# Kernel tuning notes

Measured on AMD Instinct MI355X. Metric: run time of the kernel, lower is better.

## Reference

```python
import jax, jax.numpy as jnp
import numpy as np

B, N, DIN, D, E, STEP = 4, 1024, 256, 256, 5, 5


def setup_inputs() -> dict:
    key = jax.random.key(0)
    ks = jax.random.split(key, 14)
    s = 0.02  # weight init scale
    inp = {
        "node_features": jax.random.normal(ks[0], (B, N, DIN), dtype=jnp.float32),
        # dense per-edge-type adjacency; scaled so messages stay in a sane range
        "adj_matrices": jax.random.uniform(ks[1], (B, E, N, N), dtype=jnp.float32) * (2.0 / N),
        "fc_in_w": jax.random.normal(ks[2], (D, DIN), dtype=jnp.float32) * s,
        "fc_in_b": jnp.zeros((D,), dtype=jnp.float32),
        "edge_w": jax.random.normal(ks[3], (E, D, D), dtype=jnp.float32) * s,
        "edge_b": jax.random.normal(ks[4], (E, D), dtype=jnp.float32) * s,
        "gru_w_ih": jax.random.normal(ks[5], (3 * D, D), dtype=jnp.float32) * s,
        "gru_w_hh": jax.random.normal(ks[6], (3 * D, D), dtype=jnp.float32) * s,
        "gru_b_ih": jnp.zeros((3 * D,), dtype=jnp.float32),
        "gru_b_hh": jnp.zeros((3 * D,), dtype=jnp.float32),
        "conv1_w": jax.random.normal(ks[7], (D, D), dtype=jnp.float32) * s,
        "conv1_b": jnp.zeros((D,), dtype=jnp.float32),
        "conv2_w": jax.random.normal(ks[8], (D, D), dtype=jnp.float32) * s,
        "conv2_b": jnp.zeros((D,), dtype=jnp.float32),
    }
    return inp


def _gru_cell(x, h, w_ih, w_hh, b_ih, b_hh):
    # torch GRUCell: gates ordered [r, z, n]
    gi = x @ w_ih.T + b_ih  # [B*N, 3D]
    gh = h @ w_hh.T + b_hh
    ir, iz, inn = jnp.split(gi, 3, axis=-1)
    hr, hz, hn = jnp.split(gh, 3, axis=-1)
    r = jax.nn.sigmoid(ir + hr)
    z = jax.nn.sigmoid(iz + hz)
    n = jnp.tanh(inn + r * hn)
    return (1.0 - z) * n + z * h


def reference(node_features, adj_matrices, fc_in_w, fc_in_b, edge_w, edge_b,
              gru_w_ih, gru_w_hh, gru_b_ih, gru_b_hh,
              conv1_w, conv1_b, conv2_w, conv2_b):
    h = node_features @ fc_in_w.T + fc_in_b  # [B, N, D]
    sum_edge_b = jnp.sum(edge_b, axis=0)  # accumulated biases over edge types
    for _ in range(STEP):
        # messages per edge type: adj_e @ h  -> [B, E, N, D]
        msgs = jnp.einsum('benm,bmd->bend', adj_matrices, h)
        # per-edge-type linear (y = x @ W_e.T) then accumulate over edge types
        acc = jnp.einsum('bend,ekd->bnk', msgs, edge_w) + sum_edge_b  # [B, N, D]
        h = _gru_cell(acc, h, gru_w_ih, gru_w_hh, gru_b_ih, gru_b_hh)
    node_states = h  # [B, N, D]
    # conv1d with kernel_size=1 over node axis == per-node linear on channels
    attn_weights = jax.nn.sigmoid(node_states @ conv1_w.T + conv1_b)  # [B, N, D]
    feats = jnp.tanh(node_states @ conv2_w.T + conv2_b)  # [B, N, D]
    graph_embedding = jnp.sum(attn_weights * feats, axis=1)  # sum over nodes -> [B, D]
    attn_map = jnp.mean(attn_weights, axis=2)  # mean over channels -> [B, N]
    return (graph_embedding, node_states, attn_map)
```

## Files before the change

kernel.cpp:

```cpp
#include <hip/hip_runtime.h>
#include <hip/hip_bf16.h>
#include <cstdint>


typedef __attribute__((ext_vector_type(8))) short bf16x8;
typedef __attribute__((ext_vector_type(4))) float f32x4;

__device__ __forceinline__ float bf2f(__hip_bfloat16 x) { return __bfloat162float(x); }
__device__ __forceinline__ __hip_bfloat16 f2bf(float x) { return __float2bfloat16(x); }
__device__ __forceinline__ short f2bs(float x) {
  __hip_bfloat16 h = __float2bfloat16(x);
  return *reinterpret_cast<short*>(&h);
}
__device__ __forceinline__ float s2f(short x) {
  __hip_bfloat16 h = *reinterpret_cast<__hip_bfloat16*>(&x);
  return __bfloat162float(h);
}

__device__ __forceinline__ bf16x8 ld8_ext(const void* base, long off, bool f32) {
  if (f32) {
    const float* p = (const float*)base + off;
    bf16x8 r;
#pragma unroll
    for (int i = 0; i < 8; ++i) r[i] = f2bs(p[i]);
    return r;
  }
  return *(const bf16x8*)((const __hip_bfloat16*)base + off);
}

__device__ __forceinline__ bf16x8 ld8_sum5(const __hip_bfloat16* part, int row, int k) {
  const long base = (long)row * 256 + (long)(row >> 10) * 1048576 + k;
  float s[8] = {0.f, 0.f, 0.f, 0.f, 0.f, 0.f, 0.f, 0.f};
#pragma unroll
  for (int e = 0; e < 5; ++e) {
    bf16x8 v = *(const bf16x8*)(part + base + e * 262144);
#pragma unroll
    for (int j = 0; j < 8; ++j) s[j] += s2f(v[j]);
  }
  bf16x8 r;
#pragma unroll
  for (int j = 0; j < 8; ++j) r[j] = f2bs(s[j]);
  return r;
}

__global__ void detect_dtype(const uint32_t* __restrict__ raw, int* __restrict__ flag) {
  __shared__ int cnt;
  if (threadIdx.x == 0) cnt = 0;
  __syncthreads();
  int c = 0;
  for (int i = threadIdx.x; i < 512; i += 256) {
    uint32_t byte = (raw[i] >> 8) & 0xFF;
    if (byte >= 0x28 && byte <= 0x40) ++c;
  }
  atomicAdd(&cnt, c);
  __syncthreads();
  if (threadIdx.x == 0) *flag = (cnt < 300) ? 1 : 0;
}

__global__ void prep_pool(const void* fcb, const void* bih, const void* bhh,
                          const void* c1b, const void* c2b, const void* edgeb,
                          const int* __restrict__ flag,
                          float* __restrict__ pool, float* __restrict__ ge,
                          float* __restrict__ am32) {
  const bool f32 = (*flag != 0);
  for (int t = threadIdx.x; t < 2560; t += 256) {
    const void* p; int i;
    if (t < 256)       { p = fcb;  i = t; }
    else if (t < 1024) { p = bih;  i = t - 256; }
    else if (t < 1792) { p = bhh;  i = t - 1024; }
    else if (t < 2048) { p = c1b;  i = t - 1792; }
    else if (t < 2304) { p = c2b;  i = t - 2048; }
    else {
      int k = t - 2304; float s = 0.f;
      for (int e = 0; e < 5; ++e)
        s += f32 ? ((const float*)edgeb)[e * 256 + k]
                 : bf2f(((const __hip_bfloat16*)edgeb)[e * 256 + k]);
      pool[t] = s; continue;
    }
    pool[t] = f32 ? ((const float*)p)[i] : bf2f(((const __hip_bfloat16*)p)[i]);
  }
  for (int t = threadIdx.x; t < 1024; t += 256) ge[t] = 0.f;
  for (int t = threadIdx.x; t < 4096; t += 256) am32[t] = 0.f;
}

__global__ void bias_gi_k(const float* __restrict__ pool,
                          const __hip_bfloat16* __restrict__ wih,
                          float* __restrict__ out) {
  const int n = blockIdx.x * 256 + threadIdx.x;
  if (n >= 768) return;
  float s = pool[256 + n];
  for (int k = 0; k < 256; ++k) s += pool[2304 + k] * bf2f(wih[n * 256 + k]);
  out[n] = s;
}

__global__ void wcvt_all(const void* fcw, const void* edw, const void* wih,
                         const void* whh, const void* c1w, const void* c2w,
                         const int* __restrict__ flag, __hip_bfloat16* __restrict__ dst) {
  const bool f32 = (*flag != 0);
  const int i = blockIdx.x * 256 + threadIdx.x;
  const void* src; int off;
  if      (i < 65536)  { src = fcw; off = i; }
  else if (i < 393216) { src = edw; off = i - 65536; }
  else if (i < 589824) { src = wih; off = i - 393216; }
  else if (i < 786432) { src = whh; off = i - 589824; }
  else if (i < 851968) { src = c1w; off = i - 786432; }
  else                 { src = c2w; off = i - 851968; }
  dst[i] = f32 ? f2bf(((const float*)src)[off])
               : ((const __hip_bfloat16*)src)[off];
}

__global__ void adj_cvt(const void* __restrict__ src, const int* __restrict__ flag,
                        __hip_bfloat16* __restrict__ dst) {
  const bool f32 = (*flag != 0);
  const long i = ((long)blockIdx.x * 256 + threadIdx.x) * 8;
  bf16x8 r;
  if (f32) {
    const float* p = (const float*)src + i;
#pragma unroll
    for (int j = 0; j < 8; ++j) r[j] = f2bs(p[j]);
  } else {
    r = *(const bf16x8*)((const __hip_bfloat16*)src + i);
  }
  *(bf16x8*)(dst + i) = r;
}

__global__ void sum_part(const __hip_bfloat16* __restrict__ part,
                         __hip_bfloat16* __restrict__ out) {
  const int t = blockIdx.x * 256 + threadIdx.x;
  const int row = t >> 5;
  const int k = (t & 31) * 8;
  const long base = (long)row * 256 + (long)(row >> 10) * 1048576 + k;
  float s[8] = {0.f, 0.f, 0.f, 0.f, 0.f, 0.f, 0.f, 0.f};
#pragma unroll
  for (int e = 0; e < 5; ++e) {
    bf16x8 v = *(const bf16x8*)(part + base + e * 262144);
#pragma unroll
    for (int j = 0; j < 8; ++j) s[j] += s2f(v[j]);
  }
  bf16x8 r;
#pragma unroll
  for (int j = 0; j < 8; ++j) r[j] = f2bs(s[j]);
  *(bf16x8*)(out + (long)row * 256 + k) = r;
}

template<bool HAS_BIAS, bool DUAL>
__global__ __launch_bounds__(256)
void gemm_bt128(const __hip_bfloat16* __restrict__ A, const __hip_bfloat16* __restrict__ Bt,
                const float* __restrict__ bias, __hip_bfloat16* __restrict__ C,
                const __hip_bfloat16* __restrict__ A2, const __hip_bfloat16* __restrict__ Bt2,
                const float* __restrict__ bias2, __hip_bfloat16* __restrict__ C2,
                int K, int lda, int ldb, int ldc,
                long aBatch, int zdivA, int zmodA,
                long bBatch, int zdivB, int zmodB,
                long cBatch, int zdivC, int zSplit)
{
  __shared__ __align__(16) __hip_bfloat16 sA[128 * 64];
  __shared__ __align__(16) __hip_bfloat16 sB[64 * 64];
  const int t = threadIdx.x;
  const int w = t >> 6;
  const int l = t & 63;
  const int m0 = blockIdx.x * 128;
  const int n0 = blockIdx.y * 64;
  int z = blockIdx.z;

  const __hip_bfloat16* Au = A; const __hip_bfloat16* Btu = Bt;
  const float* biasu = bias; __hip_bfloat16* Cu = C;
  if (DUAL && z >= zSplit) { Au = A2; Btu = Bt2; biasu = bias2; Cu = C2; z -= zSplit; }

  const __hip_bfloat16* Ab = Au + (long)((z / zdivA) % zmodA) * aBatch;
  const __hip_bfloat16* Bb = Btu + (long)((z / zdivB) % zmodB) * bBatch;

  int sra[4], sca[4];
#pragma unroll
  for (int i = 0; i < 4; ++i) {
    const int p = t + 256 * i;
    sra[i] = p >> 3;
    sca[i] = (p & 7) ^ (sra[i] & 7);
  }
  const int p0 = t, p1 = t + 256;
  const int sr0 = p0 >> 3, sc0 = (p0 & 7) ^ (sr0 & 7);
  const int sr1 = p1 >> 3, sc1 = (p1 & 7) ^ (sr1 & 7);

  f32x4 acc[2][4];
#pragma unroll
  for (int i = 0; i < 2; ++i)
#pragma unroll
    for (int j = 0; j < 4; ++j) acc[i][j] = (f32x4){0.f, 0.f, 0.f, 0.f};

  const int r15 = l & 15;
  const int quad = l >> 4;

  for (int k0 = 0; k0 < K; k0 += 64) {
    bf16x8 av[4];
#pragma unroll
    for (int i = 0; i < 4; ++i)
      av[i] = *(const bf16x8*)(Ab + (long)(m0 + sra[i]) * lda + (k0 + sca[i] * 8));
    bf16x8 b0 = *(const bf16x8*)(Bb + (long)(n0 + sr0) * ldb + (k0 + sc0 * 8));
    bf16x8 b1 = *(const bf16x8*)(Bb + (long)(n0 + sr1) * ldb + (k0 + sc1 * 8));
    __syncthreads();
#pragma unroll
    for (int i = 0; i < 4; ++i) *(bf16x8*)(sA + (t + 256 * i) * 8) = av[i];
    *(bf16x8*)(sB + p0 * 8) = b0;
    *(bf16x8*)(sB + p1 * 8) = b1;
    __syncthreads();
#pragma unroll
    for (int ks = 0; ks < 2; ++ks) {
      const int cg = ks * 4 + quad;
      bf16x8 aF[2], bF[4];
#pragma unroll
      for (int mi = 0; mi < 2; ++mi) {
        const int row = mi * 64 + w * 16 + r15;
        aF[mi] = *(const bf16x8*)(sA + row * 64 + ((cg ^ (row & 7)) * 8));
      }
#pragma unroll
      for (int ni = 0; ni < 4; ++ni) {
        const int nrow = ni * 16 + r15;
        bF[ni] = *(const bf16x8*)(sB + nrow * 64 + ((cg ^ (nrow & 7)) * 8));
      }
#pragma unroll
      for (int mi = 0; mi < 2; ++mi)
#pragma unroll
        for (int ni = 0; ni < 4; ++ni)
          acc[mi][ni] = __builtin_amdgcn_mfma_f32_16x16x32_bf16(
              aF[mi], bF[ni], acc[mi][ni], 0, 0, 0);
    }
  }

  const long cOff = (long)(z / zdivC) * cBatch;
#pragma unroll
  for (int mi = 0; mi < 2; ++mi) {
#pragma unroll
    for (int ni = 0; ni < 4; ++ni) {
      const int n = n0 + ni * 16 + r15;
      float bv = 0.f;
      if (HAS_BIAS) bv = biasu[n];
#pragma unroll
      for (int r = 0; r < 4; ++r) {
        const int m = m0 + mi * 64 + w * 16 + quad * 4 + r;
        Cu[cOff + (long)m * ldc + n] = f2bf(acc[mi][ni][r] + bv);
      }
    }
  }
}

template<int OUT_MODE, bool HAS_BIAS, int A_MODE, bool DUAL>
__global__ __launch_bounds__(256)
void gemm_bt(const void* __restrict__ A, const __hip_bfloat16* __restrict__ Bt,
             const float* __restrict__ bias, void* __restrict__ Cp,
             const void* __restrict__ A2, const __hip_bfloat16* __restrict__ Bt2,
             const float* __restrict__ bias2, void* __restrict__ Cp2,
             const int* __restrict__ flag,
             int Kg, int ngrp, int lda, int ldb, int ldc,
             long aBatch, int zdivA, int zmodA,
             long bBatch, int zdivB, int zmodB,
             long cBatch, int zdivC, long aGrp, long bGrp, int zSplit)
{
  __shared__ __align__(16) __hip_bfloat16 sA[64 * 64];
  __shared__ __align__(16) __hip_bfloat16 sB[64 * 64];
  const bool af32 = (A_MODE == 1) ? (*flag != 0) : false;
  const int t = threadIdx.x;
  const int w = t >> 6;
  const int l = t & 63;
  const int m0 = blockIdx.x * 64;
  const int n0 = blockIdx.y * 64;
  int z = blockIdx.z;

  const void* Au = A; const __hip_bfloat16* Btu = Bt;
  const float* biasu = bias; void* Cpu = Cp;
  bool second = false;
  if (DUAL && z >= zSplit) {
    Au = A2; Btu = Bt2; biasu = bias2; Cpu = Cp2; z -= zSplit; second = true;
  }

  const long aOff = (long)((z / zdivA) % zmodA) * aBatch;
  const __hip_bfloat16* Bb = Btu + (long)((z / zdivB) % zmodB) * bBatch;

  const int p0 = t, p1 = t + 256;
  const int sr0 = p0 >> 3, sc0 = (p0 & 7) ^ (sr0 & 7);
  const int sr1 = p1 >> 3, sc1 = (p1 & 7) ^ (sr1 & 7);

  f32x4 acc[4];
#pragma unroll
  for (int i = 0; i < 4; ++i) acc[i] = (f32x4){0.f, 0.f, 0.f, 0.f};

  const int mrow = w * 16 + (l & 15);
  const int quad = l >> 4;

  for (int g = 0; g < ngrp; ++g) {
    const long aG = aOff + (long)g * aGrp;
    const __hip_bfloat16* Bg = Bb + (long)g * bGrp;
    for (int k0 = 0; k0 < Kg; k0 += 64) {
      bf16x8 a0, a1;
      if (A_MODE == 2 && !second) {
        a0 = ld8_sum5((const __hip_bfloat16*)Au, m0 + sr0, k0 + sc0 * 8);
        a1 = ld8_sum5((const __hip_bfloat16*)Au, m0 + sr1, k0 + sc1 * 8);
      } else if (A_MODE == 1) {
        a0 = ld8_ext(Au, aG + (long)(m0 + sr0) * lda + (k0 + sc0 * 8), af32);
        a1 = ld8_ext(Au, aG + (long)(m0 + sr1) * lda + (k0 + sc1 * 8), af32);
      } else {
        const __hip_bfloat16* Ab = (const __hip_bfloat16*)Au;
        a0 = *(const bf16x8*)(Ab + aG + (long)(m0 + sr0) * lda + (k0 + sc0 * 8));
        a1 = *(const bf16x8*)(Ab + aG + (long)(m0 + sr1) * lda + (k0 + sc1 * 8));
      }
      bf16x8 b0 = *(const bf16x8*)(Bg + (long)(n0 + sr0) * ldb + (k0 + sc0 * 8));
      bf16x8 b1 = *(const bf16x8*)(Bg + (long)(n0 + sr1) * ldb + (k0 + sc1 * 8));
      __syncthreads();
      *(bf16x8*)(sA + p0 * 8) = a0;
      *(bf16x8*)(sA + p1 * 8) = a1;
      *(bf16x8*)(sB + p0 * 8) = b0;
      *(bf16x8*)(sB + p1 * 8) = b1;
      __syncthreads();
#pragma unroll
      for (int ks = 0; ks < 2; ++ks) {
        const int cg = ks * 4 + quad;
        bf16x8 af = *(const bf16x8*)(sA + mrow * 64 + ((cg ^ (mrow & 7)) * 8));
#pragma unroll
        for (int t4 = 0; t4 < 4; ++t4) {
          const int nrow = t4 * 16 + (l & 15);
          bf16x8 bfr = *(const bf16x8*)(sB + nrow * 64 + ((cg ^ (nrow & 7)) * 8));
          acc[t4] = __builtin_amdgcn_mfma_f32_16x16x32_bf16(af, bfr, acc[t4], 0, 0, 0);
        }
      }
    }
  }

  const long cOff = (long)(z / zdivC) * cBatch;
#pragma unroll
  for (int t4 = 0; t4 < 4; ++t4) {
    const int n = n0 + t4 * 16 + (l & 15);
    float bv = 0.f;
    if (HAS_BIAS) bv = biasu[n];
#pragma unroll
    for (int r = 0; r < 4; ++r) {
      const int m = m0 + w * 16 + quad * 4 + r;
      const float v = acc[t4][r] + bv;
      if (OUT_MODE == 0)
        ((__hip_bfloat16*)Cpu)[cOff + (long)m * ldc + n] = f2bf(v);
      else
        ((float*)Cpu)[cOff + (long)m * ldc + n] = v;
    }
  }
}

__global__ void gru_gate8(const __hip_bfloat16* __restrict__ gi,
                          const __hip_bfloat16* __restrict__ gh,
                          __hip_bfloat16* __restrict__ hbf,
                          void* __restrict__ ns_out, const int* __restrict__ flag)
{
  const int t = blockIdx.x * 256 + threadIdx.x;
  const int m = t >> 5;
  const int k = (t & 31) * 8;
  const long gb = (long)m * 768 + k;
  bf16x8 vir = *(const bf16x8*)(gi + gb);
  bf16x8 viz = *(const bf16x8*)(gi + gb + 256);
  bf16x8 vin = *(const bf16x8*)(gi + gb + 512);
  bf16x8 vhr = *(const bf16x8*)(gh + gb);
  bf16x8 vhz = *(const bf16x8*)(gh + gb + 256);
  bf16x8 vhn = *(const bf16x8*)(gh + gb + 512);
  const long hidx = (long)m * 256 + k;
  bf16x8 vh = *(const bf16x8*)(hbf + hidx);
  bf16x8 out;
  float hf[8];
#pragma unroll
  for (int j = 0; j < 8; ++j) {
    const float r = 1.f / (1.f + __expf(-(s2f(vir[j]) + s2f(vhr[j]))));
    const float zz = 1.f / (1.f + __expf(-(s2f(viz[j]) + s2f(vhz[j]))));
    const float nn = tanhf(s2f(vin[j]) + r * s2f(vhn[j]));
    hf[j] = (1.f - zz) * nn + zz * s2f(vh[j]);
    out[j] = f2bs(hf[j]);
  }
  *(bf16x8*)(hbf + hidx) = out;
  if (ns_out) {
    if (*flag) {
      float* o = (float*)ns_out + 1024 + hidx;
#pragma unroll
      for (int j = 0; j < 8; ++j) o[j] = hf[j];
    } else {
      *(bf16x8*)((__hip_bfloat16*)ns_out + 1024 + hidx) = out;
    }
  }
}

__global__ __launch_bounds__(256)
void conv_fused(const __hip_bfloat16* __restrict__ hbf,
                const __hip_bfloat16* __restrict__ c1w,
                const __hip_bfloat16* __restrict__ c2w,
                const float* __restrict__ pool,
                float* __restrict__ geg, float* __restrict__ am32)
{
  __shared__ __align__(16) __hip_bfloat16 sA[64 * 64];
  __shared__ __align__(16) __hip_bfloat16 sB1[64 * 64];
  __shared__ __align__(16) __hip_bfloat16 sB2[64 * 64];
  __shared__ float sge[64];
  __shared__ float sam[64];
  const int t = threadIdx.x, w = t >> 6, l = t & 63;
  const int m0 = blockIdx.x * 64, n0 = blockIdx.y * 64;
  if (t < 64) { sge[t] = 0.f; sam[t] = 0.f; }
  const int p0 = t, p1 = t + 256;
  const int sr0 = p0 >> 3, sc0 = (p0 & 7) ^ (sr0 & 7);
  const int sr1 = p1 >> 3, sc1 = (p1 & 7) ^ (sr1 & 7);
  f32x4 a1[4], a2[4];
#pragma unroll
  for (int i = 0; i < 4; ++i) { a1[i] = (f32x4){0,0,0,0}; a2[i] = (f32x4){0,0,0,0}; }
  const int mrow = w * 16 + (l & 15);
  const int quad = l >> 4;
  for (int k0 = 0; k0 < 256; k0 += 64) {
    bf16x8 va0 = *(const bf16x8*)(hbf + (long)(m0 + sr0) * 256 + (k0 + sc0 * 8));
    bf16x8 va1 = *(const bf16x8*)(hbf + (long)(m0 + sr1) * 256 + (k0 + sc1 * 8));
    bf16x8 vb0 = *(const bf16x8*)(c1w + (long)(n0 + sr0) * 256 + (k0 + sc0 * 8));
    bf16x8 vb1 = *(const bf16x8*)(c1w + (long)(n0 + sr1) * 256 + (k0 + sc1 * 8));
    bf16x8 vc0 = *(const bf16x8*)(c2w + (long)(n0 + sr0) * 256 + (k0 + sc0 * 8));
    bf16x8 vc1 = *(const bf16x8*)(c2w + (long)(n0 + sr1) * 256 + (k0 + sc1 * 8));
    __syncthreads();
    *(bf16x8*)(sA + p0 * 8) = va0;  *(bf16x8*)(sA + p1 * 8) = va1;
    *(bf16x8*)(sB1 + p0 * 8) = vb0; *(bf16x8*)(sB1 + p1 * 8) = vb1;
    *(bf16x8*)(sB2 + p0 * 8) = vc0; *(bf16x8*)(sB2 + p1 * 8) = vc1;
    __syncthreads();
#pragma unroll
    for (int ks = 0; ks < 2; ++ks) {
      const int cg = ks * 4 + quad;
      bf16x8 af = *(const bf16x8*)(sA + mrow * 64 + ((cg ^ (mrow & 7)) * 8));
#pragma unroll
      for (int t4 = 0; t4 < 4; ++t4) {
        const int nrow = t4 * 16 + (l & 15);
        bf16x8 b1f = *(const bf16x8*)(sB1 + nrow * 64 + ((cg ^ (nrow & 7)) * 8));
        bf16x8 b2f = *(const bf16x8*)(sB2 + nrow * 64 + ((cg ^ (nrow & 7)) * 8));
        a1[t4] = __builtin_amdgcn_mfma_f32_16x16x32_bf16(af, b1f, a1[t4], 0, 0, 0);
        a2[t4] = __builtin_amdgcn_mfma_f32_16x16x32_bf16(af, b2f, a2[t4], 0, 0, 0);
      }
    }
  }
  float asum[4] = {0.f, 0.f, 0.f, 0.f};
#pragma unroll
  for (int t4 = 0; t4 < 4; ++t4) {
    const int n = n0 + t4 * 16 + (l & 15);
    const float bb1 = pool[1792 + n], bb2 = pool[2048 + n];
    float g = 0.f;
#pragma unroll
    for (int r = 0; r < 4; ++r) {
      const float av = 1.f / (1.f + __expf(-(a1[t4][r] + bb1)));
      const float fv = tanhf(a2[t4][r] + bb2);
      g += av * fv;
      asum[r] += av;
    }
    atomicAdd(&sge[t4 * 16 + (l & 15)], g);
  }
#pragma unroll
  for (int r = 0; r < 4; ++r) atomicAdd(&sam[w * 16 + quad * 4 + r], asum[r]);
  __syncthreads();
  if (t < 64) atomicAdd(&geg[(m0 >> 10) * 256 + n0 + t], sge[t]);
  else if (t < 128) atomicAdd(&am32[m0 + (t - 64)], sam[t - 64]);
}

__global__ void finish_out(const float* __restrict__ ge, const float* __restrict__ am32,
                           void* __restrict__ dout, const int* __restrict__ flag)
{
  const int t = blockIdx.x * 256 + threadIdx.x;
  const bool f32 = (*flag != 0);
  if (t < 1024) {
    if (f32) ((float*)dout)[t] = ge[t];
    else     ((__hip_bfloat16*)dout)[t] = f2bf(ge[t]);
  } else {
    const float v = am32[t - 1024] * (1.f / 256.f);
    if (f32) ((float*)dout)[1049600 + t - 1024] = v;
    else     ((__hip_bfloat16*)dout)[1049600 + t - 1024] = f2bf(v);
  }
}

extern "C" void kernel_launch(void* const* d_in, const int* in_sizes, int n_in,
                              void* d_out, int out_size, void* d_ws, size_t ws_size,
                              hipStream_t stream) {
  (void)in_sizes; (void)n_in; (void)out_size;
  const void* node_f = d_in[0];
  const void* adj    = d_in[1];
  const void* fc_w   = d_in[2];
  const void* fc_b   = d_in[3];
  const void* edge_w = d_in[4];
  const void* edge_b = d_in[5];
  const void* w_ih   = d_in[6];
  const void* w_hh   = d_in[7];
  const void* b_ih   = d_in[8];
  const void* b_hh   = d_in[9];
  const void* c1w    = d_in[10];
  const void* c1b    = d_in[11];
  const void* c2w    = d_in[12];
  const void* c2b    = d_in[13];

  char* ws = (char*)d_ws;
  const size_t MB = (size_t)1 << 20;
  int*            flag = (int*)(ws);
  float*          bp   = (float*)(ws + 256);
  float*          ge   = (float*)(ws + 14336);
  float*          am32 = (float*)(ws + 18432);
  __hip_bfloat16* wbf  = (__hip_bfloat16*)(ws + 34816);
  __hip_bfloat16* hbf  = (__hip_bfloat16*)(ws + 1869824);
  char*           S    = ws + 3966976;
  __hip_bfloat16* heT  = (__hip_bfloat16*)(S);
  __hip_bfloat16* part = (__hip_bfloat16*)(S + 10 * MB);
  __hip_bfloat16* gi   = (__hip_bfloat16*)(S + 20 * MB);
  __hip_bfloat16* gh   = (__hip_bfloat16*)(S + 26 * MB);
  __hip_bfloat16* spt  = (__hip_bfloat16*)(S + 32 * MB);
  __hip_bfloat16* adjb = (__hip_bfloat16*)(ws + 40 * MB);

  const bool has_split = ws_size >= 38 * MB;
  const bool has_adjb  = ws_size >= 81 * MB;

  detect_dtype<<<1, 256, 0, stream>>>((const uint32_t*)adj, flag);
  prep_pool<<<1, 256, 0, stream>>>(fc_b, b_ih, b_hh, c1b, c2b, edge_b, flag, bp, ge, am32);
  wcvt_all<<<3584, 256, 0, stream>>>(fc_w, edge_w, w_ih, w_hh, c1w, c2w, flag, wbf);
  bias_gi_k<<<3, 256, 0, stream>>>(bp, wbf + 393216, bp + 2560);
  if (has_adjb) adj_cvt<<<10240, 256, 0, stream>>>(adj, flag, adjb);

  gemm_bt<0, true, 1, false><<<dim3(64, 4, 1), 256, 0, stream>>>(
      node_f, wbf + 0, bp + 0, hbf, nullptr, nullptr, nullptr, nullptr, flag,
      256, 1, 256, 256, 256, 0, 1, 1, 0, 1, 1, 0, 1, 0, 0, 0);

  for (int s = 0; s < 5; ++s) {
    if (has_adjb) {
      gemm_bt128<false, false><<<dim3(2, 16, 20), 256, 0, stream>>>(
          wbf + 65536, hbf, nullptr, heT, nullptr, nullptr, nullptr, nullptr,
          256, 256, 256, 1024,
          65536, 1, 5,
          262144, 5, 4,
          262144, 1, 0);
      gemm_bt128<false, false><<<dim3(8, 4, 20), 256, 0, stream>>>(
          adjb, heT, nullptr, part, nullptr, nullptr, nullptr, nullptr,
          1024, 1024, 1024, 256,
          1048576, 1, 20,
          262144, 1, 20,
          262144, 1, 0);
      sum_part<<<512, 256, 0, stream>>>(part, spt);
      gemm_bt128<true, true><<<dim3(32, 12, 2), 256, 0, stream>>>(
          spt, wbf + 393216, bp + 2560, gi,
          hbf, wbf + 589824, bp + 1024, gh,
          256, 256, 256, 768,
          0, 1, 1, 0, 1, 1, 0, 1, 1);
    } else if (has_split) {
      gemm_bt<0, false, 0, false><<<dim3(4, 16, 20), 256, 0, stream>>>(
          wbf + 65536, hbf, nullptr, heT, nullptr, nullptr, nullptr, nullptr, flag,
          256, 1, 256, 256, 1024,
          65536, 1, 5, 262144, 5, 4,
          262144, 1, 0, 0, 0);
      gemm_bt<0, false, 1, false><<<dim3(16, 4, 20), 256, 0, stream>>>(
          adj, heT, nullptr, part, nullptr, nullptr, nullptr, nullptr, flag,
          1024, 1, 1024, 1024, 256,
          1048576, 1, 20, 262144, 1, 20,
          262144, 1, 0, 0, 0);
      gemm_bt<0, true, 2, true><<<dim3(64, 12, 2), 256, 0, stream>>>(
          part, wbf + 393216, bp + 2560, gi,
          hbf,  wbf + 589824, bp + 1024, gh, flag,
          256, 1, 256, 256, 768, 0, 1, 1, 0, 1, 1, 0, 1, 0, 0, 1);
    } else {
      gemm_bt<0, false, 0, false><<<dim3(4, 16, 20), 256, 0, stream>>>(
          wbf + 65536, hbf, nullptr, heT, nullptr, nullptr, nullptr, nullptr, flag,
          256, 1, 256, 256, 1024,
          65536, 1, 5, 262144, 5, 4,
          262144, 1, 0, 0, 0);
      gemm_bt<0, true, 1, false><<<dim3(16, 4, 4), 256, 0, stream>>>(
          adj, heT, bp + 2304, part, nullptr, nullptr, nullptr, nullptr, flag,
          1024, 5, 1024, 1024, 256,
          (long)5 * 1048576, 1, 4, (long)5 * 262144, 1, 4,
          262144, 1, 1048576, 262144, 0);
      gemm_bt<0, true, 0, true><<<dim3(64, 12, 2), 256, 0, stream>>>(
          part, wbf + 393216, bp + 256, gi,
          hbf,  wbf + 589824, bp + 1024, gh, flag,
          256, 1, 256, 256, 768, 0, 1, 1, 0, 1, 1, 0, 1, 0, 0, 1);
    }
    gru_gate8<<<512, 256, 0, stream>>>(gi, gh, hbf,
                                       (s == 4) ? d_out : nullptr, flag);
  }

  conv_fused<<<dim3(64, 4), 256, 0, stream>>>(hbf, wbf + 786432, wbf + 851968,
                                              bp, ge, am32);
  finish_out<<<20, 256, 0, stream>>>(ge, am32, d_out, flag);
}
```

Baseline: 449.3 us.

## Fuse partial-sum into gi GEMM with GRU gate, co-schedule adjacency and gh GEMMs

In the adjacency-converted path, the adjacency GEMM and the h·W_hh GEMM now run in one launch that splits blocks by index. A new gi_gate kernel sums the five edge-type partials as it loads them (ld8_sum5), computes all three gate projections per tile, and applies the GRU update in its epilogue. This drops the sum_part kernel, the intermediate spt and gi buffers, and the separate gru_gate8 launch. The cost is more shared memory and accumulators per block in gi_gate and only 256 blocks for that stage, which may limit occupancy.

```diff
diff --git a/kernel.cpp b/kernel.cpp
--- a/kernel.cpp
+++ b/kernel.cpp
@@ -124,25 +124,6 @@
   *(bf16x8*)(dst + i) = r;
 }
 
-__global__ void sum_part(const __hip_bfloat16* __restrict__ part,
-                         __hip_bfloat16* __restrict__ out) {
-  const int t = blockIdx.x * 256 + threadIdx.x;
-  const int row = t >> 5;
-  const int k = (t & 31) * 8;
-  const long base = (long)row * 256 + (long)(row >> 10) * 1048576 + k;
-  float s[8] = {0.f, 0.f, 0.f, 0.f, 0.f, 0.f, 0.f, 0.f};
-#pragma unroll
-  for (int e = 0; e < 5; ++e) {
-    bf16x8 v = *(const bf16x8*)(part + base + e * 262144);
-#pragma unroll
-    for (int j = 0; j < 8; ++j) s[j] += s2f(v[j]);
-  }
-  bf16x8 r;
-#pragma unroll
-  for (int j = 0; j < 8; ++j) r[j] = f2bs(s[j]);
-  *(bf16x8*)(out + (long)row * 256 + k) = r;
-}
-
 template<bool HAS_BIAS, bool DUAL>
 __global__ __launch_bounds__(256)
 void gemm_bt128(const __hip_bfloat16* __restrict__ A, const __hip_bfloat16* __restrict__ Bt,
@@ -238,6 +219,212 @@
       for (int r = 0; r < 4; ++r) {
         const int m = m0 + mi * 64 + w * 16 + quad * 4 + r;
         Cu[cOff + (long)m * ldc + n] = f2bf(acc[mi][ni][r] + bv);
+      }
+    }
+  }
+}
+
+__global__ __launch_bounds__(256)
+void part_gh(const __hip_bfloat16* __restrict__ adjb,
+             const __hip_bfloat16* __restrict__ heT,
+             __hip_bfloat16* __restrict__ part,
+             const __hip_bfloat16* __restrict__ hbf,
+             const __hip_bfloat16* __restrict__ whh,
+             const float* __restrict__ bhh,
+             __hip_bfloat16* __restrict__ gh)
+{
+  __shared__ __align__(16) __hip_bfloat16 sA[128 * 64];
+  __shared__ __align__(16) __hip_bfloat16 sB[64 * 64];
+  const int t = threadIdx.x;
+  const int w = t >> 6;
+  const int l = t & 63;
+  const int bid = blockIdx.x;
+
+  const __hip_bfloat16* Ab; const __hip_bfloat16* Bb;
+  __hip_bfloat16* Cu; const float* biasu = nullptr;
+  int K, lda, ldb, ldc, m0, n0;
+  bool has_bias;
+  if (bid < 640) {
+    const int z = bid >> 5, rem = bid & 31;
+    m0 = (rem & 7) * 128; n0 = (rem >> 3) * 64;
+    Ab = adjb + (long)z * 1048576; lda = 1024; K = 1024;
+    Bb = heT + (long)z * 262144;  ldb = 1024;
+    Cu = part + (long)z * 262144; ldc = 256;
+    has_bias = false;
+  } else {
+    const int idx = bid - 640;
+    m0 = (idx & 31) * 128; n0 = (idx >> 5) * 64;
+    Ab = hbf; lda = 256; K = 256;
+    Bb = whh; ldb = 256;
+    Cu = gh;  ldc = 768;
+    biasu = bhh; has_bias = true;
+  }
+
+  int sra[4], sca[4];
+#pragma unroll
+  for (int i = 0; i < 4; ++i) {
+    const int p = t + 256 * i;
+    sra[i] = p >> 3;
+    sca[i] = (p & 7) ^ (sra[i] & 7);
+  }
+  const int p0 = t, p1 = t + 256;
+  const int sr0 = p0 >> 3, sc0 = (p0 & 7) ^ (sr0 & 7);
+  const int sr1 = p1 >> 3, sc1 = (p1 & 7) ^ (sr1 & 7);
+
+  f32x4 acc[2][4];
+#pragma unroll
+  for (int i = 0; i < 2; ++i)
+#pragma unroll
+    for (int j = 0; j < 4; ++j) acc[i][j] = (f32x4){0.f, 0.f, 0.f, 0.f};
+
+  const int r15 = l & 15;
+  const int quad = l >> 4;
+
+  for (int k0 = 0; k0 < K; k0 += 64) {
+    bf16x8 av[4];
+#pragma unroll
+    for (int i = 0; i < 4; ++i)
+      av[i] = *(const bf16x8*)(Ab + (long)(m0 + sra[i]) * lda + (k0 + sca[i] * 8));
+    bf16x8 b0 = *(const bf16x8*)(Bb + (long)(n0 + sr0) * ldb + (k0 + sc0 * 8));
+    bf16x8 b1 = *(const bf16x8*)(Bb + (long)(n0 + sr1) * ldb + (k0 + sc1 * 8));
+    __syncthreads();
+#pragma unroll
+    for (int i = 0; i < 4; ++i) *(bf16x8*)(sA + (t + 256 * i) * 8) = av[i];
+    *(bf16x8*)(sB + p0 * 8) = b0;
+    *(bf16x8*)(sB + p1 * 8) = b1;
+    __syncthreads();
+#pragma unroll
+    for (int ks = 0; ks < 2; ++ks) {
+      const int cg = ks * 4 + quad;
+      bf16x8 aF[2], bF[4];
+#pragma unroll
+      for (int mi = 0; mi < 2; ++mi) {
+        const int row = mi * 64 + w * 16 + r15;
+        aF[mi] = *(const bf16x8*)(sA + row * 64 + ((cg ^ (row & 7)) * 8));
+      }
+#pragma unroll
+      for (int ni = 0; ni < 4; ++ni) {
+        const int nrow = ni * 16 + r15;
+        bF[ni] = *(const bf16x8*)(sB + nrow * 64 + ((cg ^ (nrow & 7)) * 8));
+      }
+#pragma unroll
+      for (int mi = 0; mi < 2; ++mi)
+#pragma unroll
+        for (int ni = 0; ni < 4; ++ni)
+          acc[mi][ni] = __builtin_amdgcn_mfma_f32_16x16x32_bf16(
+              aF[mi], bF[ni], acc[mi][ni], 0, 0, 0);
+    }
+  }
+
+#pragma unroll
+  for (int mi = 0; mi < 2; ++mi) {
+#pragma unroll
+    for (int ni = 0; ni < 4; ++ni) {
+      const int n = n0 + ni * 16 + r15;
+      const float bv = has_bias ? biasu[n] : 0.f;
+#pragma unroll
+      for (int r = 0; r < 4; ++r) {
+        const int m = m0 + mi * 64 + w * 16 + quad * 4 + r;
+        Cu[(long)m * ldc + n] = f2bf(acc[mi][ni][r] + bv);
+      }
+    }
+  }
+}
+
+__global__ __launch_bounds__(256)
+void gi_gate(const __hip_bfloat16* __restrict__ part,
+             const __hip_bfloat16* __restrict__ wih,
+             const float* __restrict__ biasgi,
+             const __hip_bfloat16* __restrict__ gh,
+             __hip_bfloat16* __restrict__ hbf,
+             void* __restrict__ ns_out, const int* __restrict__ flag)
+{
+  __shared__ __align__(16) __hip_bfloat16 sA[64 * 64];
+  __shared__ __align__(16) __hip_bfloat16 sB0[64 * 64];
+  __shared__ __align__(16) __hip_bfloat16 sB1[64 * 64];
+  __shared__ __align__(16) __hip_bfloat16 sB2[64 * 64];
+  const int t = threadIdx.x;
+  const int w = t >> 6;
+  const int l = t & 63;
+  const int m0 = (blockIdx.x & 63) * 64;
+  const int n0 = (blockIdx.x >> 6) * 64;
+
+  const int p0 = t, p1 = t + 256;
+  const int sr0 = p0 >> 3, sc0 = (p0 & 7) ^ (sr0 & 7);
+  const int sr1 = p1 >> 3, sc1 = (p1 & 7) ^ (sr1 & 7);
+
+  f32x4 acc[3][4];
+#pragma unroll
+  for (int g = 0; g < 3; ++g)
+#pragma unroll
+    for (int j = 0; j < 4; ++j) acc[g][j] = (f32x4){0.f, 0.f, 0.f, 0.f};
+
+  const int mrow = w * 16 + (l & 15);
+  const int r15 = l & 15;
+  const int quad = l >> 4;
+
+  for (int k0 = 0; k0 < 256; k0 += 64) {
+    bf16x8 a0 = ld8_sum5(part, m0 + sr0, k0 + sc0 * 8);
+    bf16x8 a1 = ld8_sum5(part, m0 + sr1, k0 + sc1 * 8);
+    bf16x8 bg[3][2];
+#pragma unroll
+    for (int g = 0; g < 3; ++g) {
+      bg[g][0] = *(const bf16x8*)(wih + (long)(g * 256 + n0 + sr0) * 256 + (k0 + sc0 * 8));
+      bg[g][1] = *(const bf16x8*)(wih + (long)(g * 256 + n0 + sr1) * 256 + (k0 + sc1 * 8));
+    }
+    __syncthreads();
+    *(bf16x8*)(sA + p0 * 8) = a0;
+    *(bf16x8*)(sA + p1 * 8) = a1;
+    *(bf16x8*)(sB0 + p0 * 8) = bg[0][0]; *(bf16x8*)(sB0 + p1 * 8) = bg[0][1];
+    *(bf16x8*)(sB1 + p0 * 8) = bg[1][0]; *(bf16x8*)(sB1 + p1 * 8) = bg[1][1];
+    *(bf16x8*)(sB2 + p0 * 8) = bg[2][0]; *(bf16x8*)(sB2 + p1 * 8) = bg[2][1];
+    __syncthreads();
+#pragma unroll
+    for (int ks = 0; ks < 2; ++ks) {
+      const int cg = ks * 4 + quad;
+      bf16x8 af = *(const bf16x8*)(sA + mrow * 64 + ((cg ^ (mrow & 7)) * 8));
+#pragma unroll
+      for (int t4 = 0; t4 < 4; ++t4) {
+        const int nrow = t4 * 16 + r15;
+        const int so = nrow * 64 + ((cg ^ (nrow & 7)) * 8);
+        bf16x8 b0f = *(const bf16x8*)(sB0 + so);
+        bf16x8 b1f = *(const bf16x8*)(sB1 + so);
+        bf16x8 b2f = *(const bf16x8*)(sB2 + so);
+        acc[0][t4] = __builtin_amdgcn_mfma_f32_16x16x32_bf16(af, b0f, acc[0][t4], 0, 0, 0);
+        acc[1][t4] = __builtin_amdgcn_mfma_f32_16x16x32_bf16(af, b1f, acc[1][t4], 0, 0, 0);
+        acc[2][t4] = __builtin_amdgcn_mfma_f32_16x16x32_bf16(af, b2f, acc[2][t4], 0, 0, 0);
+      }
+    }
+  }
+
+  const bool f32out = ns_out && (*flag != 0);
+#pragma unroll
+  for (int t4 = 0; t4 < 4; ++t4) {
+    const int n = n0 + t4 * 16 + r15;
+    const float bgr = biasgi[n];
+    const float bgz = biasgi[256 + n];
+    const float bgn = biasgi[512 + n];
+#pragma unroll
+    for (int r = 0; r < 4; ++r) {
+      const int m = m0 + w * 16 + quad * 4 + r;
+      const long gb = (long)m * 768;
+      const float ir = acc[0][t4][r] + bgr;
+      const float iz = acc[1][t4][r] + bgz;
+      const float inn = acc[2][t4][r] + bgn;
+      const float hr = bf2f(gh[gb + n]);
+      const float hz = bf2f(gh[gb + 256 + n]);
+      const float hn = bf2f(gh[gb + 512 + n]);
+      const long hidx = (long)m * 256 + n;
+      const float h = bf2f(hbf[hidx]);
+      const float rr = 1.f / (1.f + __expf(-(ir + hr)));
+      const float zz = 1.f / (1.f + __expf(-(iz + hz)));
+      const float nn = tanhf(inn + rr * hn);
+      const float hnew = (1.f - zz) * nn + zz * h;
+      const __hip_bfloat16 hb = f2bf(hnew);
+      hbf[hidx] = hb;
+      if (ns_out) {
+        if (f32out) ((float*)ns_out)[1024 + hidx] = hnew;
+        else        ((__hip_bfloat16*)ns_out)[1024 + hidx] = hb;
       }
     }
   }
@@ -499,7 +686,6 @@
   __hip_bfloat16* part = (__hip_bfloat16*)(S + 10 * MB);
   __hip_bfloat16* gi   = (__hip_bfloat16*)(S + 20 * MB);
   __hip_bfloat16* gh   = (__hip_bfloat16*)(S + 26 * MB);
-  __hip_bfloat16* spt  = (__hip_bfloat16*)(S + 32 * MB);
   __hip_bfloat16* adjb = (__hip_bfloat16*)(ws + 40 * MB);
 
   const bool has_split = ws_size >= 38 * MB;
@@ -523,18 +709,10 @@
           65536, 1, 5,
           262144, 5, 4,
           262144, 1, 0);
-      gemm_bt128<false, false><<<dim3(8, 4, 20), 256, 0, stream>>>(
-          adjb, heT, nullptr, part, nullptr, nullptr, nullptr, nullptr,
-          1024, 1024, 1024, 256,
-          1048576, 1, 20,
-          262144, 1, 20,
-          262144, 1, 0);
-      sum_part<<<512, 256, 0, stream>>>(part, spt);
-      gemm_bt128<true, true><<<dim3(32, 12, 2), 256, 0, stream>>>(
-          spt, wbf + 393216, bp + 2560, gi,
-          hbf, wbf + 589824, bp + 1024, gh,
-          256, 256, 256, 768,
-          0, 1, 1, 0, 1, 1, 0, 1, 1);
+      part_gh<<<1024, 256, 0, stream>>>(adjb, heT, part,
+                                        hbf, wbf + 589824, bp + 1024, gh);
+      gi_gate<<<256, 256, 0, stream>>>(part, wbf + 393216, bp + 2560, gh, hbf,
+                                       (s == 4) ? d_out : nullptr, flag);
     } else if (has_split) {
       gemm_bt<0, false, 0, false><<<dim3(4, 16, 20), 256, 0, stream>>>(
           wbf + 65536, hbf, nullptr, heT, nullptr, nullptr, nullptr, nullptr, flag,
@@ -550,6 +728,8 @@
           part, wbf + 393216, bp + 2560, gi,
           hbf,  wbf + 589824, bp + 1024, gh, flag,
           256, 1, 256, 256, 768, 0, 1, 1, 0, 1, 1, 0, 1, 0, 0, 1);
+      gru_gate8<<<512, 256, 0, stream>>>(gi, gh, hbf,
+                                         (s == 4) ? d_out : nullptr, flag);
     } else {
       gemm_bt<0, false, 0, false><<<dim3(4, 16, 20), 256, 0, stream>>>(
           wbf + 65536, hbf, nullptr, heT, nullptr, nullptr, nullptr, nullptr, flag,
@@ -565,9 +745,9 @@
           part, wbf + 393216, bp + 256, gi,
           hbf,  wbf + 589824, bp + 1024, gh, flag,
           256, 1, 256, 256, 768, 0, 1, 1, 0, 1, 1, 0, 1, 0, 0, 1);
-    }
-    gru_gate8<<<512, 256, 0, stream>>>(gi, gh, hbf,
-                                       (s == 4) ? d_out : nullptr, flag);
+      gru_gate8<<<512, 256, 0, stream>>>(gi, gh, hbf,
+                                         (s == 4) ? d_out : nullptr, flag);
+    }
   }
 
   conv_fused<<<dim3(64, 4), 256, 0, stream>>>(hbf, wbf + 786432, wbf + 851968,
```

Result: faster. 432.8 us (median of 2 runs) (-3.7%).
